# Performance work log

Measured on AMD Instinct MI355X. Metric: run time of the kernel, lower is better.

Reference implementation:

```python
import jax, jax.numpy as jnp
import numpy as np

NUM_HEADS = 8
EPS = 1e-12  # torch F.normalize default eps


def _l2_normalize(t, axis):
    n = jnp.sqrt(jnp.sum(t * t, axis=axis, keepdims=True))
    return t / jnp.maximum(n, EPS)


def setup_inputs() -> dict:
    key = jax.random.key(0)
    k1, k2, k3 = jax.random.split(key, 3)
    B, N, D = 32, 3136, 384
    x = jax.random.normal(k1, (B, N, D), dtype=jnp.float32)
    qkv_w = jax.random.normal(k2, (3 * D, D), dtype=jnp.float32) * (1.0 / np.sqrt(D))
    temperature = jnp.ones((NUM_HEADS, 1, 1), dtype=jnp.float32)
    proj_w = jax.random.normal(k3, (D, D), dtype=jnp.float32) * (1.0 / np.sqrt(D))
    proj_b = jnp.zeros((D,), dtype=jnp.float32)
    return {"x": x, "qkv_w": qkv_w, "temperature": temperature,
            "proj_w": proj_w, "proj_b": proj_b}


def reference(x, qkv_w, temperature, proj_w, proj_b):
    B, N, D = x.shape
    H = NUM_HEADS
    C = D // H
    # qkv projection (no bias), split last dim as (3, H, C) -> (3, B, H, C, N)
    qkv = jnp.einsum('bnd,ed->bne', x, qkv_w)
    qkv = qkv.reshape(B, N, 3, H, C).transpose(2, 0, 3, 4, 1)
    q, k, v = qkv[0], qkv[1], qkv[2]            # each (B, H, C, N)
    q = _l2_normalize(q, axis=-1)               # normalize over tokens N
    k = _l2_normalize(k, axis=-1)
    # cross-covariance attention: (B, H, C, C), scaled by per-head temperature
    attn = jnp.einsum('bhcn,bhdn->bhcd', q, k) * temperature
    attn = jax.nn.softmax(attn, axis=-1)
    out = jnp.einsum('bhcd,bhdn->bhcn', attn, v)  # (B, H, C, N)
    out = out.transpose(0, 3, 1, 2).reshape(B, N, D)
    return jnp.einsum('bnd,ed->bne', out, proj_w) + proj_b
```

## Files before the change

### kernel.cpp

```cpp
#include <hip/hip_runtime.h>


typedef __bf16 bf16x8 __attribute__((ext_vector_type(8)));
typedef float floatx4 __attribute__((ext_vector_type(4)));
typedef unsigned short u16;

#define B_ 32
#define N_ 3136
#define D_ 384
#define H_ 8
#define C_ 48
#define E3_ 1152
#define BN_ 100352

__device__ __forceinline__ u16 f2b(float f) {
  unsigned u = __builtin_bit_cast(unsigned, f);
  u += 0x7FFFu + ((u >> 16) & 1u);
  return (u16)(u >> 16);
}
__device__ __forceinline__ float b2f(u16 s) {
  unsigned u = ((unsigned)s) << 16;
  return __builtin_bit_cast(float, u);
}
__device__ __forceinline__ void gload16(const u16* g, u16* l) {
  __builtin_amdgcn_global_load_lds(
      (const __attribute__((address_space(1))) void*)g,
      (__attribute__((address_space(3))) void*)l, 16, 0, 0);
}

__global__ __launch_bounds__(256) void k_cvt(const float* __restrict__ in,
                                             u16* __restrict__ out, int n4) {
  int i = blockIdx.x * 256 + threadIdx.x;
  if (i < n4) {
    float4 v = ((const float4*)in)[i];
    ushort4 o;
    o.x = f2b(v.x); o.y = f2b(v.y); o.z = f2b(v.z); o.w = f2b(v.w);
    ((ushort4*)out)[i] = o;
  }
}

__global__ __launch_bounds__(256) void k_gemm_qkv(const u16* __restrict__ W,
                                                  const u16* __restrict__ X,
                                                  u16* __restrict__ O) {
  const int K = D_;
  int m0 = blockIdx.x * 128;
  int n0 = blockIdx.y * 128;
  __shared__ u16 As[128][32];
  __shared__ u16 Bs[128][32];
  int t = threadIdx.x, wid = t >> 6, lane = t & 63;
  int srow = wid * 32 + (lane >> 2);
  int scol = (lane & 3) * 8;
  int wm = (wid & 1) * 64, wn = (wid >> 1) * 64;
  int r = lane & 15, quad = lane >> 4, q8 = quad * 8;

  const u16* gA = W + (size_t)(m0 + srow) * K + scol;
  const u16* gB = X + (size_t)(n0 + srow) * K + scol;
  u16* lA0 = &As[wid * 32][0];
  u16* lA1 = &As[wid * 32 + 16][0];
  u16* lB0 = &Bs[wid * 32][0];
  u16* lB1 = &Bs[wid * 32 + 16][0];

  floatx4 acc[4][4] = {};
  for (int k0 = 0; k0 < K; k0 += 32) {
    gload16(gA + k0, lA0);
    gload16(gA + k0 + 16 * K, lA1);
    gload16(gB + k0, lB0);
    gload16(gB + k0 + 16 * K, lB1);
    __syncthreads();
    bf16x8 af[4], bf[4];
    for (int i = 0; i < 4; i++) af[i] = *(const bf16x8*)(&As[wm + i * 16 + r][q8]);
    for (int j = 0; j < 4; j++) bf[j] = *(const bf16x8*)(&Bs[wn + j * 16 + r][q8]);
    for (int i = 0; i < 4; i++)
      for (int j = 0; j < 4; j++)
        acc[i][j] = __builtin_amdgcn_mfma_f32_16x16x32_bf16(af[i], bf[j], acc[i][j], 0, 0, 0);
    __syncthreads();
  }
  for (int i = 0; i < 4; i++)
    for (int j = 0; j < 4; j++)
      for (int v = 0; v < 4; v++) {
        int rr = m0 + wm + i * 16 + quad * 4 + v;
        int cc = n0 + wn + j * 16 + r;
        O[(size_t)rr * BN_ + cc] = f2b(acc[i][j][v]);
      }
}

__global__ __launch_bounds__(256) void k_attn_s(const u16* __restrict__ QKV,
                                                float* __restrict__ S,
                                                float* __restrict__ ssq) {
  int bh = blockIdx.x, b = bh >> 3, h = bh & 7;
  int ns = blockIdx.y * 448;
  const u16* Qb = QKV + (size_t)(h * C_) * BN_ + b * N_ + ns;
  const u16* Kb = QKV + (size_t)(D_ + h * C_) * BN_ + b * N_ + ns;
  __shared__ u16 As[64][32];
  __shared__ u16 Bs[64][32];
  int t = threadIdx.x;
  int row = t >> 2, chunk = (t & 3) * 8;
  int wid = t >> 6, lane = t & 63;
  int wm = (wid & 1) * 32, wn = (wid >> 1) * 32;
  int r = lane & 15, quad = lane >> 4, q8 = quad * 8;
  float sq_acc = 0.f, sk_acc = 0.f;
  floatx4 acc[2][2] = {};
  for (int k0 = 0; k0 < 448; k0 += 32) {
    int4 va = {0, 0, 0, 0}, vb = {0, 0, 0, 0};
    if (row < 48) {
      va = *(const int4*)(Qb + (size_t)row * BN_ + k0 + chunk);
      vb = *(const int4*)(Kb + (size_t)row * BN_ + k0 + chunk);
    }
    *(int4*)(&As[row][chunk]) = va;
    *(int4*)(&Bs[row][chunk]) = vb;
    const u16* pa = (const u16*)&va;
    const u16* pb = (const u16*)&vb;
    for (int i = 0; i < 8; i++) {
      float fa = b2f(pa[i]), fb = b2f(pb[i]);
      sq_acc += fa * fa; sk_acc += fb * fb;
    }
    __syncthreads();
    bf16x8 a0 = *(const bf16x8*)(&As[wm + r][q8]);
    bf16x8 a1 = *(const bf16x8*)(&As[wm + 16 + r][q8]);
    bf16x8 b0 = *(const bf16x8*)(&Bs[wn + r][q8]);
    bf16x8 b1 = *(const bf16x8*)(&Bs[wn + 16 + r][q8]);
    acc[0][0] = __builtin_amdgcn_mfma_f32_16x16x32_bf16(a0, b0, acc[0][0], 0, 0, 0);
    acc[0][1] = __builtin_amdgcn_mfma_f32_16x16x32_bf16(a0, b1, acc[0][1], 0, 0, 0);
    acc[1][0] = __builtin_amdgcn_mfma_f32_16x16x32_bf16(a1, b0, acc[1][0], 0, 0, 0);
    acc[1][1] = __builtin_amdgcn_mfma_f32_16x16x32_bf16(a1, b1, acc[1][1], 0, 0, 0);
    __syncthreads();
  }
  sq_acc += __shfl_xor(sq_acc, 1); sq_acc += __shfl_xor(sq_acc, 2);
  sk_acc += __shfl_xor(sk_acc, 1); sk_acc += __shfl_xor(sk_acc, 2);
  if ((t & 3) == 0 && row < 48) {
    atomicAdd(&ssq[bh * 48 + row], sq_acc);
    atomicAdd(&ssq[12288 + bh * 48 + row], sk_acc);
  }
  for (int mt = 0; mt < 2; mt++)
    for (int nt = 0; nt < 2; nt++)
      for (int v = 0; v < 4; v++) {
        int rr = wm + mt * 16 + quad * 4 + v;
        int cc = wn + nt * 16 + r;
        if (rr < 48 && cc < 48)
          atomicAdd(&S[(size_t)bh * 2304 + rr * 48 + cc], acc[mt][nt][v]);
      }
}

__global__ __launch_bounds__(64) void k_softmax(const float* __restrict__ S,
                                                const float* __restrict__ ssq,
                                                const float* __restrict__ temp,
                                                float* __restrict__ attn) {
  int bh = blockIdx.x, h = bh & 7;
  int c = threadIdx.x;
  if (c >= 48) return;
  float sq = 1.f / fmaxf(sqrtf(ssq[bh * 48 + c]), 1e-12f);
  float T = temp[h];
  const float* Srow = S + (size_t)bh * 2304 + c * 48;
  float v[48];
  float mx = -1e30f;
  for (int d = 0; d < 48; d++) {
    float sk = 1.f / fmaxf(sqrtf(ssq[12288 + bh * 48 + d]), 1e-12f);
    float l = Srow[d] * sq * sk * T;
    v[d] = l;
    mx = fmaxf(mx, l);
  }
  float sum = 0.f;
  for (int d = 0; d < 48; d++) { v[d] = expf(v[d] - mx); sum += v[d]; }
  float inv = 1.f / sum;
  float* Arow = attn + (size_t)bh * 2304 + c * 48;
  for (int d = 0; d < 48; d++) Arow[d] = v[d] * inv;
}

__global__ __launch_bounds__(256) void k_attn_v(const u16* __restrict__ QKV,
                                                const float* __restrict__ attn,
                                                u16* __restrict__ outT) {
  int bh = blockIdx.y, b = bh >> 3, h = bh & 7;
  int n0 = blockIdx.x * 64;
  const u16* V = QKV + (size_t)(2 * D_ + h * C_) * BN_ + b * N_;
  __shared__ u16 Vt[64][64];
  __shared__ u16 Aw[48][64];
  int t = threadIdx.x;
  for (int i = t; i < 64 * 64 * 2 / 16; i += 256) ((int4*)Vt)[i] = int4{0, 0, 0, 0};
  for (int i = t; i < 48 * 64 * 2 / 16; i += 256) ((int4*)Aw)[i] = int4{0, 0, 0, 0};
  __syncthreads();
  for (int idx = t; idx < 768; idx += 256) {
    int d = idx >> 4, c4 = (idx & 15) * 4;
    ushort4 v = *(const ushort4*)(V + (size_t)d * BN_ + n0 + c4);
    Vt[c4 + 0][d] = v.x; Vt[c4 + 1][d] = v.y;
    Vt[c4 + 2][d] = v.z; Vt[c4 + 3][d] = v.w;
  }
  for (int i = t; i < 2304; i += 256) {
    int c = i / 48, d = i - c * 48;
    Aw[c][d] = f2b(attn[(size_t)bh * 2304 + i]);
  }
  __syncthreads();
  int wid = t >> 6, lane = t & 63;
  int r = lane & 15, quad = lane >> 4, q8 = quad * 8;
  floatx4 acc[3] = {};
  for (int ks = 0; ks < 2; ks++) {
    bf16x8 a = *(const bf16x8*)(&Vt[wid * 16 + r][ks * 32 + q8]);
    for (int nt = 0; nt < 3; nt++) {
      bf16x8 bb = *(const bf16x8*)(&Aw[nt * 16 + r][ks * 32 + q8]);
      acc[nt] = __builtin_amdgcn_mfma_f32_16x16x32_bf16(a, bb, acc[nt], 0, 0, 0);
    }
  }
  u16* Ob = outT + (size_t)(b * N_) * D_;
  for (int nt = 0; nt < 3; nt++)
    for (int j = 0; j < 4; j++) {
      int n = n0 + wid * 16 + quad * 4 + j;
      int e = h * C_ + nt * 16 + r;
      Ob[(size_t)n * D_ + e] = f2b(acc[nt][j]);
    }
}

__global__ __launch_bounds__(256) void k_gemm_proj(const u16* __restrict__ OT,
                                                   const u16* __restrict__ P,
                                                   const float* __restrict__ bias,
                                                   float* __restrict__ Y) {
  const int K = D_;
  int n0 = blockIdx.x * 128;
  int m0 = blockIdx.y * 128;
  __shared__ u16 As[128][32];
  __shared__ u16 Bs[128][32];
  int t = threadIdx.x, wid = t >> 6, lane = t & 63;
  int srow = wid * 32 + (lane >> 2);
  int scol = (lane & 3) * 8;
  int wm = (wid & 1) * 64, wn = (wid >> 1) * 64;
  int r = lane & 15, quad = lane >> 4, q8 = quad * 8;

  const u16* gA = OT + (size_t)(m0 + srow) * K + scol;
  const u16* gB = P + (size_t)(n0 + srow) * K + scol;
  u16* lA0 = &As[wid * 32][0];
  u16* lA1 = &As[wid * 32 + 16][0];
  u16* lB0 = &Bs[wid * 32][0];
  u16* lB1 = &Bs[wid * 32 + 16][0];

  floatx4 acc[4][4] = {};
  for (int k0 = 0; k0 < K; k0 += 32) {
    gload16(gA + k0, lA0);
    gload16(gA + k0 + 16 * K, lA1);
    gload16(gB + k0, lB0);
    gload16(gB + k0 + 16 * K, lB1);
    __syncthreads();
    bf16x8 af[4], bf[4];
    for (int i = 0; i < 4; i++) af[i] = *(const bf16x8*)(&As[wm + i * 16 + r][q8]);
    for (int j = 0; j < 4; j++) bf[j] = *(const bf16x8*)(&Bs[wn + j * 16 + r][q8]);
    for (int i = 0; i < 4; i++)
      for (int j = 0; j < 4; j++)
        acc[i][j] = __builtin_amdgcn_mfma_f32_16x16x32_bf16(af[i], bf[j], acc[i][j], 0, 0, 0);
    __syncthreads();
  }
  for (int i = 0; i < 4; i++)
    for (int j = 0; j < 4; j++) {
      int cc = n0 + wn + j * 16 + r;
      float bv = bias[cc];
      for (int v = 0; v < 4; v++) {
        int rr = m0 + wm + i * 16 + quad * 4 + v;
        Y[(size_t)rr * D_ + cc] = acc[i][j][v] + bv;
      }
    }
}

extern "C" void kernel_launch(void* const* d_in, const int* in_sizes, int n_in,
                              void* d_out, int out_size, void* d_ws, size_t ws_size,
                              hipStream_t stream) {
  const float* x      = (const float*)d_in[0];
  const float* qkv_w  = (const float*)d_in[1];
  const float* temp   = (const float*)d_in[2];
  const float* proj_w = (const float*)d_in[3];
  const float* proj_b = (const float*)d_in[4];
  float* out = (float*)d_out;

  char* ws = (char*)d_ws;
  u16*   qkv    = (u16*)(ws);
  u16*   xbf    = (u16*)(ws + 231211008);
  u16*   wbf    = (u16*)(ws + 308281344);
  u16*   pwbf   = (u16*)(ws + 309166080);
  float* S      = (float*)(ws + 309460992);
  float* ssq    = (float*)(ws + 311820288);
  float* attn   = (float*)(ws + 311918592);
  u16*   outT   = xbf;

  hipMemsetAsync(S, 0, 2359296 + 98304, stream);

  k_cvt<<<38535168 / 4 / 256, 256, 0, stream>>>(x, xbf, 38535168 / 4);
  k_cvt<<<442368 / 4 / 256, 256, 0, stream>>>(qkv_w, wbf, 442368 / 4);
  k_cvt<<<147456 / 4 / 256, 256, 0, stream>>>(proj_w, pwbf, 147456 / 4);

  k_gemm_qkv<<<dim3(9, 784), 256, 0, stream>>>(wbf, xbf, qkv);
  k_attn_s<<<dim3(256, 7), 256, 0, stream>>>(qkv, S, ssq);
  k_softmax<<<256, 64, 0, stream>>>(S, ssq, temp, attn);
  k_attn_v<<<dim3(49, 256), 256, 0, stream>>>(qkv, attn, outT);
  k_gemm_proj<<<dim3(3, 784), 256, 0, stream>>>(outT, pwbf, proj_b, out);
}
```

Before: 583.4 us.

## Remap GEMM blocks per XCD and replace attention atomics with split partials

The two GEMM kernels now use a 1D grid and remap block IDs so that consecutive work tiles land on the same XCD (id&7 chunking). The aim is better L2 reuse of the shared weight and activation tiles across the MI355X's eight chiplets. The attention score kernel stops using atomicAdd into zeroed buffers. It writes per-split partial S and sum-of-squares arrays, and the softmax kernel reduces these itself, which removes the memset and atomic contention. In exchange the softmax does extra reads, and the partials now reuse the xbf workspace region, which is dead at that point.

```diff
diff --git a/kernel.cpp b/kernel.cpp
--- a/kernel.cpp
+++ b/kernel.cpp
@@ -43,8 +43,10 @@
                                                   const u16* __restrict__ X,
                                                   u16* __restrict__ O) {
   const int K = D_;
-  int m0 = blockIdx.x * 128;
-  int n0 = blockIdx.y * 128;
+  int id = blockIdx.x;
+  int work = (id & 7) * 882 + (id >> 3);
+  int m0 = (work % 9) * 128;
+  int n0 = (work / 9) * 128;
   __shared__ u16 As[128][32];
   __shared__ u16 Bs[128][32];
   int t = threadIdx.x, wid = t >> 6, lane = t & 63;
@@ -85,10 +87,11 @@
 }
 
 __global__ __launch_bounds__(256) void k_attn_s(const u16* __restrict__ QKV,
-                                                float* __restrict__ S,
-                                                float* __restrict__ ssq) {
+                                                float* __restrict__ S_part,
+                                                float* __restrict__ ssq_part) {
   int bh = blockIdx.x, b = bh >> 3, h = bh & 7;
-  int ns = blockIdx.y * 448;
+  int split = blockIdx.y;
+  int ns = split * 448;
   const u16* Qb = QKV + (size_t)(h * C_) * BN_ + b * N_ + ns;
   const u16* Kb = QKV + (size_t)(D_ + h * C_) * BN_ + b * N_ + ns;
   __shared__ u16 As[64][32];
@@ -128,36 +131,48 @@
   sq_acc += __shfl_xor(sq_acc, 1); sq_acc += __shfl_xor(sq_acc, 2);
   sk_acc += __shfl_xor(sk_acc, 1); sk_acc += __shfl_xor(sk_acc, 2);
   if ((t & 3) == 0 && row < 48) {
-    atomicAdd(&ssq[bh * 48 + row], sq_acc);
-    atomicAdd(&ssq[12288 + bh * 48 + row], sk_acc);
-  }
+    ssq_part[(((size_t)split * 2 + 0) * 256 + bh) * 48 + row] = sq_acc;
+    ssq_part[(((size_t)split * 2 + 1) * 256 + bh) * 48 + row] = sk_acc;
+  }
+  float* Sp = S_part + ((size_t)split * 256 + bh) * 2304;
   for (int mt = 0; mt < 2; mt++)
     for (int nt = 0; nt < 2; nt++)
       for (int v = 0; v < 4; v++) {
         int rr = wm + mt * 16 + quad * 4 + v;
         int cc = wn + nt * 16 + r;
-        if (rr < 48 && cc < 48)
-          atomicAdd(&S[(size_t)bh * 2304 + rr * 48 + cc], acc[mt][nt][v]);
+        if (rr < 48 && cc < 48) Sp[rr * 48 + cc] = acc[mt][nt][v];
       }
 }
 
-__global__ __launch_bounds__(64) void k_softmax(const float* __restrict__ S,
-                                                const float* __restrict__ ssq,
+__global__ __launch_bounds__(64) void k_softmax(const float* __restrict__ S_part,
+                                                const float* __restrict__ ssq_part,
                                                 const float* __restrict__ temp,
                                                 float* __restrict__ attn) {
   int bh = blockIdx.x, h = bh & 7;
   int c = threadIdx.x;
+  __shared__ float skin[48];
+  float sqin = 0.f;
+  if (c < 48) {
+    float sq = 0.f, sk = 0.f;
+    for (int s = 0; s < 7; s++) {
+      sq += ssq_part[(((size_t)s * 2 + 0) * 256 + bh) * 48 + c];
+      sk += ssq_part[(((size_t)s * 2 + 1) * 256 + bh) * 48 + c];
+    }
+    sqin = 1.f / fmaxf(sqrtf(sq), 1e-12f);
+    skin[c] = 1.f / fmaxf(sqrtf(sk), 1e-12f);
+  }
+  __syncthreads();
   if (c >= 48) return;
-  float sq = 1.f / fmaxf(sqrtf(ssq[bh * 48 + c]), 1e-12f);
   float T = temp[h];
-  const float* Srow = S + (size_t)bh * 2304 + c * 48;
-  float v[48];
+  float v[48] = {};
+  for (int s = 0; s < 7; s++) {
+    const float* Srow = S_part + ((size_t)s * 256 + bh) * 2304 + c * 48;
+    for (int d = 0; d < 48; d++) v[d] += Srow[d];
+  }
   float mx = -1e30f;
   for (int d = 0; d < 48; d++) {
-    float sk = 1.f / fmaxf(sqrtf(ssq[12288 + bh * 48 + d]), 1e-12f);
-    float l = Srow[d] * sq * sk * T;
-    v[d] = l;
-    mx = fmaxf(mx, l);
+    v[d] = v[d] * sqin * skin[d] * T;
+    mx = fmaxf(mx, v[d]);
   }
   float sum = 0.f;
   for (int d = 0; d < 48; d++) { v[d] = expf(v[d] - mx); sum += v[d]; }
@@ -213,8 +228,10 @@
                                                    const float* __restrict__ bias,
                                                    float* __restrict__ Y) {
   const int K = D_;
-  int n0 = blockIdx.x * 128;
-  int m0 = blockIdx.y * 128;
+  int id = blockIdx.x;
+  int work = (id & 7) * 294 + (id >> 3);
+  int n0 = (work % 3) * 128;
+  int m0 = (work / 3) * 128;
   __shared__ u16 As[128][32];
   __shared__ u16 Bs[128][32];
   int t = threadIdx.x, wid = t >> 6, lane = t & 63;
@@ -267,24 +284,22 @@
   float* out = (float*)d_out;
 
   char* ws = (char*)d_ws;
-  u16*   qkv    = (u16*)(ws);
-  u16*   xbf    = (u16*)(ws + 231211008);
-  u16*   wbf    = (u16*)(ws + 308281344);
-  u16*   pwbf   = (u16*)(ws + 309166080);
-  float* S      = (float*)(ws + 309460992);
-  float* ssq    = (float*)(ws + 311820288);
-  float* attn   = (float*)(ws + 311918592);
-  u16*   outT   = xbf;
-
-  hipMemsetAsync(S, 0, 2359296 + 98304, stream);
+  u16*   qkv      = (u16*)(ws);
+  u16*   xbf      = (u16*)(ws + 231211008);
+  float* S_part   = (float*)(ws + 231211008);
+  float* ssq_part = (float*)(ws + 247726080);
+  u16*   outT     = xbf;
+  u16*   wbf      = (u16*)(ws + 308281344);
+  u16*   pwbf     = (u16*)(ws + 309166080);
+  float* attn     = (float*)(ws + 309460992);
 
   k_cvt<<<38535168 / 4 / 256, 256, 0, stream>>>(x, xbf, 38535168 / 4);
   k_cvt<<<442368 / 4 / 256, 256, 0, stream>>>(qkv_w, wbf, 442368 / 4);
   k_cvt<<<147456 / 4 / 256, 256, 0, stream>>>(proj_w, pwbf, 147456 / 4);
 
-  k_gemm_qkv<<<dim3(9, 784), 256, 0, stream>>>(wbf, xbf, qkv);
-  k_attn_s<<<dim3(256, 7), 256, 0, stream>>>(qkv, S, ssq);
-  k_softmax<<<256, 64, 0, stream>>>(S, ssq, temp, attn);
+  k_gemm_qkv<<<7056, 256, 0, stream>>>(wbf, xbf, qkv);
+  k_attn_s<<<dim3(256, 7), 256, 0, stream>>>(qkv, S_part, ssq_part);
+  k_softmax<<<256, 64, 0, stream>>>(S_part, ssq_part, temp, attn);
   k_attn_v<<<dim3(49, 256), 256, 0, stream>>>(qkv, attn, outT);
-  k_gemm_proj<<<dim3(3, 784), 256, 0, stream>>>(outT, pwbf, proj_b, out);
-}
+  k_gemm_proj<<<2352, 256, 0, stream>>>(outT, pwbf, proj_b, out);
+}
```

Result: no change. 585.8 us (+0.4%).
